# Kernel tuning notes

Measured on AMD Instinct MI355X. Metric: run time of the kernel, lower is better.

## Reference

```python
import jax, jax.numpy as jnp
import numpy as np

D_MODEL = 1024
NUM_HEADS = 16
HEAD_DIM = D_MODEL // NUM_HEADS
B, S = 2, 2048


def setup_inputs() -> dict:
    key = jax.random.key(0)
    ks = jax.random.split(key, 11)
    scale = 1.0 / np.sqrt(D_MODEL)
    inp = {
        "Q": jax.random.normal(ks[0], (B, S, D_MODEL), jnp.float32),
        "K": jax.random.normal(ks[1], (B, S, D_MODEL), jnp.float32),
        "V": jax.random.normal(ks[2], (B, S, D_MODEL), jnp.float32),
        # Linear weights stored as [in, out] (transposed nn.Linear layout)
        "Wq": jax.random.normal(ks[3], (D_MODEL, D_MODEL), jnp.float32) * scale,
        "bq": jax.random.normal(ks[4], (D_MODEL,), jnp.float32) * scale,
        "Wk": jax.random.normal(ks[5], (D_MODEL, D_MODEL), jnp.float32) * scale,
        "bk": jax.random.normal(ks[6], (D_MODEL,), jnp.float32) * scale,
        "Wv": jax.random.normal(ks[7], (D_MODEL, D_MODEL), jnp.float32) * scale,
        "bv": jax.random.normal(ks[8], (D_MODEL,), jnp.float32) * scale,
        "Wo": jax.random.normal(ks[9], (D_MODEL, D_MODEL), jnp.float32) * scale,
        "bo": jax.random.normal(ks[10], (D_MODEL,), jnp.float32) * scale,
    }
    return inp


def _split_heads(x):
    # [B, S, D] -> [B, H, S, Dh]
    b, s, _ = x.shape
    return x.reshape(b, s, NUM_HEADS, HEAD_DIM).transpose(0, 2, 1, 3)


def reference(Q, K, V, Wq, bq, Wk, bk, Wv, bv, Wo, bo):
    q = _split_heads(Q @ Wq + bq)   # [B,H,S,Dh]
    k = _split_heads(K @ Wk + bk)
    v = _split_heads(V @ Wv + bv)
    scores = jnp.einsum("bhqd,bhkd->bhqk", q, k) / jnp.sqrt(
        jnp.asarray(HEAD_DIM, q.dtype))
    attn = jax.nn.softmax(scores, axis=-1)
    out = jnp.einsum("bhqk,bhkd->bhqd", attn, v)  # [B,H,S,Dh]
    out = out.transpose(0, 2, 1, 3).reshape(Q.shape[0], -1, D_MODEL)
    return out @ Wo + bo
```

## Files before the change

### kernel.cpp

```cpp
#include <hip/hip_runtime.h>
#include <hip/hip_bf16.h>

typedef short bf16x4 __attribute__((ext_vector_type(4)));
typedef short bf16x8 __attribute__((ext_vector_type(8)));
typedef float fp32x4 __attribute__((ext_vector_type(4)));

#define MFMA16(a, b, c) __builtin_amdgcn_mfma_f32_16x16x32_bf16(a, b, c, 0, 0, 0)

static __device__ __forceinline__ short f2bf(float f) {
    unsigned int b = __float_as_uint(f);
    b += 0x7fffu + ((b >> 16) & 1u);
    return (short)(b >> 16);
}

__global__ __launch_bounds__(256) void transpose_w(
    const float* __restrict__ W0, const float* __restrict__ W1,
    const float* __restrict__ W2, const float* __restrict__ W3,
    short* __restrict__ wbt)
{
    __shared__ short t[64][68];
    const int tid = threadIdx.x;
    const int z = blockIdx.z;
    const float* W = (z == 0) ? W0 : (z == 1) ? W1 : (z == 2) ? W2 : W3;
    short* dst = wbt + (size_t)z * 1024 * 1024;
    const int k0 = blockIdx.x * 64, n0 = blockIdx.y * 64;

#pragma unroll
    for (int p = 0; p < 4; ++p) {
        int c = p * 256 + tid;
        int kr = c >> 4, seg = c & 15;
        fp32x4 f = *(const fp32x4*)&W[(k0 + kr) * 1024 + n0 + seg * 4];
#pragma unroll
        for (int i = 0; i < 4; ++i) t[kr][seg * 4 + i] = f2bf(f[i]);
    }
    __syncthreads();
#pragma unroll
    for (int p = 0; p < 2; ++p) {
        int c = p * 256 + tid;
        int nr = c >> 3, ks = c & 7;
        bf16x8 v;
#pragma unroll
        for (int i = 0; i < 8; ++i) v[i] = t[ks * 8 + i][nr];
        *(bf16x8*)&dst[(n0 + nr) * 1024 + k0 + ks * 8] = v;
    }
}

struct GemmArgs {
    const void* X[3];
    const short* W;
    const float* bias[3];
    void* out[3];
};

template <bool XFP32, bool HEADED>
__global__ __launch_bounds__(256) void gemm128(GemmArgs ga)
{
    __shared__ __align__(16) short lds_a[128 * 40];
    __shared__ __align__(16) short lds_b[128 * 40];

    const int tid  = threadIdx.x;
    const int lane = tid & 63;
    const int wv   = tid >> 6;
    const int l15  = lane & 15;
    const int quad = lane >> 4;
    const int wm   = (wv >> 1) * 64;
    const int wn   = (wv & 1) * 64;
    const int z    = blockIdx.z;
    const int m0   = blockIdx.y * 128;
    const int n0   = blockIdx.x * 128;

    const void*  Xv   = ga.X[z];
    const short* W    = ga.W + (size_t)z * 1024 * 1024;
    const float* bias = ga.bias[z];
    void* outv        = ga.out[z];

    fp32x4 acc[4][4];
#pragma unroll
    for (int i = 0; i < 4; ++i)
#pragma unroll
        for (int j = 0; j < 4; ++j)
#pragma unroll
            for (int r = 0; r < 4; ++r) acc[i][j][r] = 0.f;

    for (int k0 = 0; k0 < 1024; k0 += 32) {
        __syncthreads();
        if (XFP32) {
            const float* X = (const float*)Xv;
#pragma unroll
            for (int p = 0; p < 4; ++p) {
                int c = p * 256 + tid;
                int row = c >> 3, ks = c & 7;
                fp32x4 f = *(const fp32x4*)&X[(m0 + row) * 1024 + k0 + ks * 4];
                bf16x4 s;
#pragma unroll
                for (int i = 0; i < 4; ++i) s[i] = f2bf(f[i]);
                *(bf16x4*)&lds_a[row * 40 + ks * 4] = s;
            }
        } else {
            const short* X = (const short*)Xv;
#pragma unroll
            for (int p = 0; p < 2; ++p) {
                int c = p * 256 + tid;
                int row = c >> 2, ks = c & 3;
                *(bf16x8*)&lds_a[row * 40 + ks * 8] =
                    *(const bf16x8*)&X[(m0 + row) * 1024 + k0 + ks * 8];
            }
        }
#pragma unroll
        for (int p = 0; p < 2; ++p) {
            int c = p * 256 + tid;
            int row = c >> 2, ks = c & 3;
            *(bf16x8*)&lds_b[row * 40 + ks * 8] =
                *(const bf16x8*)&W[(n0 + row) * 1024 + k0 + ks * 8];
        }
        __syncthreads();

        bf16x8 af[4], bf[4];
#pragma unroll
        for (int i = 0; i < 4; ++i)
            af[i] = *(bf16x8*)&lds_a[(wm + i * 16 + l15) * 40 + quad * 8];
#pragma unroll
        for (int j = 0; j < 4; ++j)
            bf[j] = *(bf16x8*)&lds_b[(wn + j * 16 + l15) * 40 + quad * 8];
#pragma unroll
        for (int i = 0; i < 4; ++i)
#pragma unroll
            for (int j = 0; j < 4; ++j)
                acc[i][j] = MFMA16(af[i], bf[j], acc[i][j]);
    }

#pragma unroll
    for (int i = 0; i < 4; ++i)
#pragma unroll
        for (int j = 0; j < 4; ++j)
#pragma unroll
            for (int r = 0; r < 4; ++r) {
                int row = m0 + wm + i * 16 + quad * 4 + r;
                int col = n0 + wn + j * 16 + l15;
                float v = acc[i][j][r] + bias[col];
                if (HEADED) {
                    int b = row >> 11, s = row & 2047;
                    int h = col >> 6,  dh = col & 63;
                    ((short*)outv)[(((b * 16) + h) * 2048 + s) * 64 + dh] = f2bf(v);
                } else {
                    ((float*)outv)[row * 1024 + col] = v;
                }
            }
}

__global__ __launch_bounds__(256) void attention128(
    const short* __restrict__ q, const short* __restrict__ k,
    const short* __restrict__ v, short* __restrict__ ctx)
{
    __shared__ __align__(16) short lds_k[64 * 74];
    __shared__ __align__(16) short lds_vt[64 * 74];

    const int tid  = threadIdx.x;
    const int lane = tid & 63;
    const int wv   = tid >> 6;
    const int l15  = lane & 15;
    const int quad = lane >> 4;
    const int bh   = blockIdx.y;
    const int q0   = blockIdx.x * 128 + wv * 32;

    const short* qb = q + (size_t)bh * 2048 * 64;
    const short* kb = k + (size_t)bh * 2048 * 64;
    const short* vb = v + (size_t)bh * 2048 * 64;

    bf16x8 qf[2][2];
#pragma unroll
    for (int qt = 0; qt < 2; ++qt)
#pragma unroll
        for (int h2 = 0; h2 < 2; ++h2)
            qf[qt][h2] = *(const bf16x8*)
                &qb[(q0 + qt * 16 + l15) * 64 + h2 * 32 + quad * 8];

    fp32x4 O[2][4];
    fp32x4 rs4[2];
#pragma unroll
    for (int qt = 0; qt < 2; ++qt) {
#pragma unroll
        for (int g = 0; g < 4; ++g)
#pragma unroll
            for (int r = 0; r < 4; ++r) O[qt][g][r] = 0.f;
#pragma unroll
        for (int r = 0; r < 4; ++r) rs4[qt][r] = 0.f;
    }

    const float SCL2E = 0.125f * 1.44269504088896340736f;

    const int k2   = tid >> 3;
    const int seg  = tid & 7;
    const int kk0  = k2 * 2;
    const int pos0 = (kk0 & 32) + (((kk0 & 15) >> 2) << 3)
                   + (((kk0 >> 4) & 1) << 2) + (kk0 & 3);

    const int krow = tid >> 3;
    const int kseg = tid & 7;

    for (int key0 = 0; key0 < 2048; key0 += 64) {
        __syncthreads();
        *(bf16x8*)&lds_k[krow * 74 + kseg * 8] =
            *(const bf16x8*)&kb[(key0 + krow) * 64 + kseg * 8];
        *(bf16x8*)&lds_k[(krow + 32) * 74 + kseg * 8] =
            *(const bf16x8*)&kb[(key0 + krow + 32) * 64 + kseg * 8];
        bf16x8 v0 = *(const bf16x8*)&vb[(key0 + kk0) * 64 + seg * 8];
        bf16x8 v1 = *(const bf16x8*)&vb[(key0 + kk0 + 1) * 64 + seg * 8];
#pragma unroll
        for (int i = 0; i < 8; ++i) {
            unsigned int w = (unsigned int)(unsigned short)v0[i]
                           | ((unsigned int)(unsigned short)v1[i] << 16);
            *(unsigned int*)&lds_vt[(seg * 8 + i) * 74 + pos0] = w;
        }
        __syncthreads();

        bf16x8 kf[4][2];
#pragma unroll
        for (int kc = 0; kc < 4; ++kc)
#pragma unroll
            for (int h2 = 0; h2 < 2; ++h2)
                kf[kc][h2] = *(bf16x8*)
                    &lds_k[(kc * 16 + l15) * 74 + h2 * 32 + quad * 8];

        bf16x8 pfr[2][2];
#pragma unroll
        for (int qt = 0; qt < 2; ++qt) {
#pragma unroll
            for (int kc = 0; kc < 4; ++kc) {
                fp32x4 s;
#pragma unroll
                for (int r = 0; r < 4; ++r) s[r] = 0.f;
                s = MFMA16(kf[kc][0], qf[qt][0], s);
                s = MFMA16(kf[kc][1], qf[qt][1], s);
#pragma unroll
                for (int r = 0; r < 4; ++r) {
                    float p = __builtin_amdgcn_exp2f(s[r] * SCL2E);
                    rs4[qt][r] += p;
                    pfr[qt][kc >> 1][(kc & 1) * 4 + r] = f2bf(p);
                }
            }
        }

#pragma unroll
        for (int g = 0; g < 4; ++g)
#pragma unroll
            for (int ks = 0; ks < 2; ++ks) {
                bf16x8 vf = *(bf16x8*)
                    &lds_vt[(g * 16 + l15) * 74 + ks * 32 + quad * 8];
#pragma unroll
                for (int qt = 0; qt < 2; ++qt)
                    O[qt][g] = MFMA16(pfr[qt][ks], vf, O[qt][g]);
            }
    }

    const int b = bh >> 4, h = bh & 15;
#pragma unroll
    for (int qt = 0; qt < 2; ++qt) {
        float t = (rs4[qt][0] + rs4[qt][1]) + (rs4[qt][2] + rs4[qt][3]);
        t += __shfl_xor(t, 16);
        t += __shfl_xor(t, 32);
#pragma unroll
        for (int r = 0; r < 4; ++r) {
            float tot = __shfl(t, quad * 4 + r);
            float inv = 1.f / tot;
            int qq  = q0 + qt * 16 + quad * 4 + r;
            int row = b * 2048 + qq;
#pragma unroll
            for (int g = 0; g < 4; ++g) {
                int col = h * 64 + g * 16 + l15;
                ctx[row * 1024 + col] = f2bf(O[qt][g][r] * inv);
            }
        }
    }
}

extern "C" void kernel_launch(void* const* d_in, const int* in_sizes, int n_in,
                              void* d_out, int out_size, void* d_ws, size_t ws_size,
                              hipStream_t stream) {
    const float* Q  = (const float*)d_in[0];
    const float* K  = (const float*)d_in[1];
    const float* V  = (const float*)d_in[2];
    const float* Wq = (const float*)d_in[3];
    const float* bq = (const float*)d_in[4];
    const float* Wk = (const float*)d_in[5];
    const float* bk = (const float*)d_in[6];
    const float* Wv = (const float*)d_in[7];
    const float* bv = (const float*)d_in[8];
    const float* Wo = (const float*)d_in[9];
    const float* bo = (const float*)d_in[10];

    const size_t NEL = 4096ull * 1024ull;
    short* wbt  = (short*)d_ws;
    short* vbuf = wbt + 4 * 1024 * 1024;
    short* cbuf = vbuf + NEL;
    short* qbuf = (short*)d_out;
    short* kbuf = (short*)d_out + NEL;

    dim3 blk(256);
    hipLaunchKernelGGL(transpose_w, dim3(16, 16, 4), blk, 0, stream,
                       Wq, Wk, Wv, Wo, wbt);

    GemmArgs g1;
    g1.X[0] = Q;  g1.X[1] = K;  g1.X[2] = V;
    g1.W = wbt;
    g1.bias[0] = bq; g1.bias[1] = bk; g1.bias[2] = bv;
    g1.out[0] = qbuf; g1.out[1] = kbuf; g1.out[2] = vbuf;
    hipLaunchKernelGGL((gemm128<true, true>), dim3(8, 32, 3), blk, 0, stream, g1);

    hipLaunchKernelGGL(attention128, dim3(16, 32), blk, 0, stream,
                       qbuf, kbuf, vbuf, cbuf);

    GemmArgs g2;
    g2.X[0] = cbuf; g2.X[1] = cbuf; g2.X[2] = cbuf;
    g2.W = wbt + 3ull * 1024 * 1024;
    g2.bias[0] = bo; g2.bias[1] = bo; g2.bias[2] = bo;
    g2.out[0] = d_out; g2.out[1] = d_out; g2.out[2] = d_out;
    hipLaunchKernelGGL((gemm128<false, false>), dim3(8, 32, 1), blk, 0, stream, g2);
}
```

Before: 269.3 us.

## Double-buffer K/V tiles in attention with register prefetch two chunks ahead

The attention kernel now keeps two LDS buffers for the K and transposed V tiles. Global loads for chunk t+2 are issued into registers while chunk t is computed, and chunk t+1 is written to the other LDS buffer. This cuts one barrier per iteration and hides global load latency behind the MFMA work. The cost is double the LDS footprint (about 37KB) and extra registers, which may lower occupancy.

```diff
diff --git a/kernel.cpp b/kernel.cpp
--- a/kernel.cpp
+++ b/kernel.cpp
@@ -152,8 +152,8 @@
     const short* __restrict__ q, const short* __restrict__ k,
     const short* __restrict__ v, short* __restrict__ ctx)
 {
-    __shared__ __align__(16) short lds_k[64 * 74];
-    __shared__ __align__(16) short lds_vt[64 * 74];
+    __shared__ __align__(16) short lds_k[2][64 * 74];
+    __shared__ __align__(16) short lds_vt[2][64 * 74];
 
     const int tid  = threadIdx.x;
     const int lane = tid & 63;
@@ -189,38 +189,55 @@
 
     const float SCL2E = 0.125f * 1.44269504088896340736f;
 
-    const int k2   = tid >> 3;
+    const int krow = tid >> 3;
+    const int kseg = tid & 7;
+    const int kk0  = (tid >> 3) * 2;
     const int seg  = tid & 7;
-    const int kk0  = k2 * 2;
     const int pos0 = (kk0 & 32) + (((kk0 & 15) >> 2) << 3)
                    + (((kk0 >> 4) & 1) << 2) + (kk0 & 3);
 
-    const int krow = tid >> 3;
-    const int kseg = tid & 7;
-
-    for (int key0 = 0; key0 < 2048; key0 += 64) {
-        __syncthreads();
-        *(bf16x8*)&lds_k[krow * 74 + kseg * 8] =
-            *(const bf16x8*)&kb[(key0 + krow) * 64 + kseg * 8];
-        *(bf16x8*)&lds_k[(krow + 32) * 74 + kseg * 8] =
-            *(const bf16x8*)&kb[(key0 + krow + 32) * 64 + kseg * 8];
-        bf16x8 v0 = *(const bf16x8*)&vb[(key0 + kk0) * 64 + seg * 8];
-        bf16x8 v1 = *(const bf16x8*)&vb[(key0 + kk0 + 1) * 64 + seg * 8];
-#pragma unroll
-        for (int i = 0; i < 8; ++i) {
-            unsigned int w = (unsigned int)(unsigned short)v0[i]
-                           | ((unsigned int)(unsigned short)v1[i] << 16);
-            *(unsigned int*)&lds_vt[(seg * 8 + i) * 74 + pos0] = w;
-        }
-        __syncthreads();
+    bf16x8 rk0, rk1, rv0, rv1;
+
+#define LOADCH(key0)                                                         \
+    do {                                                                     \
+        rk0 = *(const bf16x8*)&kb[((key0) + krow) * 64 + kseg * 8];          \
+        rk1 = *(const bf16x8*)&kb[((key0) + krow + 32) * 64 + kseg * 8];     \
+        rv0 = *(const bf16x8*)&vb[((key0) + kk0) * 64 + seg * 8];            \
+        rv1 = *(const bf16x8*)&vb[((key0) + kk0 + 1) * 64 + seg * 8];        \
+    } while (0)
+
+#define WRITECH(bf_)                                                         \
+    do {                                                                     \
+        *(bf16x8*)&lds_k[bf_][krow * 74 + kseg * 8] = rk0;                   \
+        *(bf16x8*)&lds_k[bf_][(krow + 32) * 74 + kseg * 8] = rk1;            \
+        _Pragma("unroll")                                                    \
+        for (int i_ = 0; i_ < 8; ++i_) {                                     \
+            unsigned int w_ = (unsigned int)(unsigned short)rv0[i_]          \
+                            | ((unsigned int)(unsigned short)rv1[i_] << 16); \
+            *(unsigned int*)&lds_vt[bf_][(seg * 8 + i_) * 74 + pos0] = w_;   \
+        }                                                                    \
+    } while (0)
+
+    LOADCH(0);
+    WRITECH(0);
+    LOADCH(64);
+    __syncthreads();
+
+    for (int t = 0; t < 32; ++t) {
+        const int cur = t & 1;
+        if (t + 1 < 32) WRITECH((t + 1) & 1);
+        if (t + 2 < 32) LOADCH((t + 2) * 64);
+
+        const short* lk = lds_k[cur];
+        const short* lv = lds_vt[cur];
 
         bf16x8 kf[4][2];
 #pragma unroll
         for (int kc = 0; kc < 4; ++kc)
 #pragma unroll
             for (int h2 = 0; h2 < 2; ++h2)
-                kf[kc][h2] = *(bf16x8*)
-                    &lds_k[(kc * 16 + l15) * 74 + h2 * 32 + quad * 8];
+                kf[kc][h2] = *(const bf16x8*)
+                    &lk[(kc * 16 + l15) * 74 + h2 * 32 + quad * 8];
 
         bf16x8 pfr[2][2];
 #pragma unroll
@@ -245,13 +262,17 @@
         for (int g = 0; g < 4; ++g)
 #pragma unroll
             for (int ks = 0; ks < 2; ++ks) {
-                bf16x8 vf = *(bf16x8*)
-                    &lds_vt[(g * 16 + l15) * 74 + ks * 32 + quad * 8];
+                bf16x8 vf = *(const bf16x8*)
+                    &lv[(g * 16 + l15) * 74 + ks * 32 + quad * 8];
 #pragma unroll
                 for (int qt = 0; qt < 2; ++qt)
                     O[qt][g] = MFMA16(pfr[qt][ks], vf, O[qt][g]);
             }
-    }
+
+        __syncthreads();
+    }
+#undef LOADCH
+#undef WRITECH
 
     const int b = bh >> 4, h = bh & 15;
 #pragma unroll
```

Result: slower. 324.4 us (+20.5%).
